# Performance work log

Hardware: AMD Instinct MI355X
Metric: run time of the kernel (lower is better)

## Reference

```python
import jax, jax.numpy as jnp
import numpy as np

B, T, D, V, L = 16, 1024, 512, 5000, 128
BLANK = 0
NEG = -1e30  # log-space 'zero' (avoid inf for stability)


def setup_inputs() -> dict:
    key = jax.random.key(0)
    k1, k2, k3, k4, k5 = jax.random.split(key, 5)
    hs_pad = jax.random.normal(k1, (B, T, D), jnp.float32)
    W = jax.random.normal(k2, (D, V), jnp.float32) * 0.02
    b = jnp.zeros((V,), jnp.float32)
    hlens = jax.random.randint(k3, (B,), T // 2, T + 1)          # frame lengths
    ys_lens = jax.random.randint(k4, (B,), 64, L + 1)             # label lengths
    ys_pad = jax.random.randint(k5, (B, L), 1, V)                 # labels, no blank
    return {"hs_pad": hs_pad, "hlens": hlens, "ys_pad": ys_pad,
            "ys_lens": ys_lens, "W": W, "b": b}


def _lse3(a, b, c):
    m = jnp.maximum(jnp.maximum(a, b), c)
    m = jnp.maximum(m, NEG)
    return m + jnp.log(jnp.exp(a - m) + jnp.exp(b - m) + jnp.exp(c - m))


def _ctc_loss(logp, hlens, ys_pad, ys_lens):
    # logp: (B, T, V) log-probabilities
    Bb, Tt, _ = logp.shape
    Ll = ys_pad.shape[1]
    S = 2 * Ll + 1
    # extended label sequence: blank, y1, blank, y2, ..., blank  -> (B, S)
    ext = jnp.full((Bb, S), BLANK, ys_pad.dtype).at[:, 1::2].set(ys_pad)
    # gather log-probs of extended labels: (B, T, S)
    lp_ext = jnp.take_along_axis(
        logp, jnp.broadcast_to(ext[:, None, :], (Bb, Tt, S)), axis=2)
    # skip transition from s-2 allowed iff ext[s] != blank and ext[s] != ext[s-2]
    ext_m2 = jnp.pad(ext[:, :-2], ((0, 0), (2, 0)), constant_values=-1)
    allow = (ext != BLANK) & (ext != ext_m2)  # (B, S)

    alpha0 = (jnp.full((Bb, S), NEG, logp.dtype)
              .at[:, 0].set(lp_ext[:, 0, 0])
              .at[:, 1].set(lp_ext[:, 0, 1]))

    def step(alpha, xs):
        lp_t, t = xs
        a1 = alpha
        a2 = jnp.pad(alpha[:, :-1], ((0, 0), (1, 0)), constant_values=NEG)
        a3 = jnp.where(allow,
                       jnp.pad(alpha[:, :-2], ((0, 0), (2, 0)), constant_values=NEG),
                       NEG)
        new = _lse3(a1, a2, a3) + lp_t
        keep = (t < hlens)[:, None]  # freeze alpha past each sequence length
        return jnp.where(keep, new, alpha), None

    lp_seq = jnp.swapaxes(lp_ext, 0, 1)  # (T, B, S)
    ts = jnp.arange(1, Tt)
    alpha, _ = jax.lax.scan(step, alpha0, (lp_seq[1:], ts))

    idx1 = 2 * ys_lens                 # final blank
    idx2 = jnp.maximum(idx1 - 1, 0)    # final label
    a_end = jnp.take_along_axis(alpha, jnp.stack([idx1, idx2], axis=1), axis=1)
    ll = jax.scipy.special.logsumexp(a_end, axis=1)  # (B,)
    loss = -ll
    loss = jnp.where(jnp.isfinite(loss) & (loss < 1e29), loss, 0.0)  # zero_infinity
    # reduction='sum', then normalize by total token count (normalize_length=True)
    return jnp.sum(loss) / jnp.sum(ys_lens).astype(logp.dtype)


def reference(hs_pad, hlens, ys_pad, ys_lens, W, b):
    logits = hs_pad @ W + b                      # (B, T, V), dropout_rate=0
    logp = jax.nn.log_softmax(logits, axis=2)    # same math as transpose->log_softmax
    return _ctc_loss(logp, hlens, ys_pad, ys_lens)
```

## Files before the change

### kernel.cpp

```cpp
#include <hip/hip_runtime.h>
#include <hip/hip_bf16.h>
#include <math.h>

#define B_   16
#define T_   1024
#define D_   512
#define V_   5000
#define VP_  5120
#define L_   128
#define S_   257
#define J_   129
#define JP_  160
#define M_   (B_*T_)
#define NT_  40
#define NEGF (-1e30f)
#define LOG2E_F 1.4426950408889634f

typedef __attribute__((ext_vector_type(8))) short short8;
typedef __attribute__((ext_vector_type(4))) float float4v;

__device__ inline void load_lds_16(const void* g, void* l) {
    __builtin_amdgcn_global_load_lds(
        (const __attribute__((address_space(1))) unsigned int*)g,
        (__attribute__((address_space(3))) unsigned int*)l, 16, 0, 0);
}

__device__ inline unsigned short f2bf(float f) {
    union { float f; unsigned int u; } x; x.f = f;
    unsigned int r = x.u + 0x7FFFu + ((x.u >> 16) & 1u);
    return (unsigned short)(r >> 16);
}

__device__ inline float wave_shr1_f32(float v) {
    return __int_as_float(__builtin_amdgcn_update_dpp(
        0, __float_as_int(v), 0x138, 0xF, 0xF, true));
}
__device__ inline int wave_shr1_i32(int v) {
    return __builtin_amdgcn_update_dpp(0, v, 0x138, 0xF, 0xF, true);
}

__global__ __launch_bounds__(256) void k_convert_hs(
    const float* __restrict__ hs, unsigned short* __restrict__ Ah)
{
    size_t base = ((size_t)blockIdx.x * 256 + threadIdx.x) * 8;
    float4 a = *(const float4*)&hs[base];
    float4 b = *(const float4*)&hs[base + 4];
    short8 o;
    o[0] = (short)f2bf(a.x); o[1] = (short)f2bf(a.y);
    o[2] = (short)f2bf(a.z); o[3] = (short)f2bf(a.w);
    o[4] = (short)f2bf(b.x); o[5] = (short)f2bf(b.y);
    o[6] = (short)f2bf(b.z); o[7] = (short)f2bf(b.w);
    *(short8*)&Ah[base] = o;
}

__global__ __launch_bounds__(256) void k_transpose_w(
    const float* __restrict__ W, unsigned short* __restrict__ Wt)
{
    __shared__ float tile[32][33];
    int v0 = blockIdx.x * 32, k0 = blockIdx.y * 32;
    int tx = threadIdx.x, ty = threadIdx.y;
#pragma unroll
    for (int r = 0; r < 4; r++) {
        int kk = r * 8 + ty;
        float val = 0.f;
        if (v0 + tx < V_) val = W[(size_t)(k0 + kk) * V_ + v0 + tx];
        tile[kk][tx] = val;
    }
    __syncthreads();
#pragma unroll
    for (int r = 0; r < 4; r++) {
        int vloc = r * 8 + ty;
        Wt[(size_t)(v0 + vloc) * D_ + k0 + tx] = f2bf(tile[tx][vloc]);
    }
}

__global__ __launch_bounds__(512) void k_gemm_lse_mfma(
    const unsigned short* __restrict__ Ah,
    const unsigned short* __restrict__ Wt,
    const float* __restrict__ bias,
    float* __restrict__ part_s)
{
    __shared__ unsigned short As[256 * 32];
    __shared__ unsigned short Bs[128 * 32];
    __shared__ float sm_s[2][256];

    const int bx = blockIdx.x;
    const int by = blockIdx.y;
    const int tid = threadIdx.x;
    const int rowBase = bx * 256, colBase = by * 128;
    const int lane = tid & 63, wv = tid >> 6;
    const int wi = wv >> 1, wj = wv & 1;
    const int g = lane >> 4, lo = lane & 15;
    const int cs = g ^ (lo & 3);

    float4v acc[4][4];
#pragma unroll
    for (int i = 0; i < 4; i++)
#pragma unroll
        for (int j = 0; j < 4; j++) acc[i][j] = (float4v){0.f, 0.f, 0.f, 0.f};

    for (int it = 0; it < 16; it++) {
        const int k0 = it * 32;
        __syncthreads();
#pragma unroll
        for (int l = 0; l < 3; l++) {
            int slot = tid + l * 512;
            if (slot < 1024) {
                int r = slot >> 2, q = slot & 3;
                int qs = q ^ (r & 3);
                load_lds_16(&Ah[(size_t)(rowBase + r) * D_ + k0 + qs * 8],
                            &As[r * 32 + q * 8]);
            } else {
                int s = slot - 1024;
                int r = s >> 2, q = s & 3;
                int qs = q ^ (r & 3);
                load_lds_16(&Wt[(size_t)(colBase + r) * D_ + k0 + qs * 8],
                            &Bs[r * 32 + q * 8]);
            }
        }
        __syncthreads();

        short8 a[4], b[4];
#pragma unroll
        for (int i = 0; i < 4; i++)
            a[i] = *(const short8*)&As[(wi * 64 + i * 16 + lo) * 32 + cs * 8];
#pragma unroll
        for (int j = 0; j < 4; j++)
            b[j] = *(const short8*)&Bs[(wj * 64 + j * 16 + lo) * 32 + cs * 8];
#pragma unroll
        for (int i = 0; i < 4; i++)
#pragma unroll
            for (int j = 0; j < 4; j++)
                acc[i][j] = __builtin_amdgcn_mfma_f32_16x16x32_bf16(
                    a[i], b[j], acc[i][j], 0, 0, 0);
    }

    float bj[4]; bool vj[4];
#pragma unroll
    for (int j = 0; j < 4; j++) {
        int col = colBase + wj * 64 + j * 16 + lo;
        vj[j] = (col < V_);
        bj[j] = vj[j] ? bias[col] : 0.f;
    }
#pragma unroll
    for (int i = 0; i < 4; i++) {
#pragma unroll
        for (int r = 0; r < 4; r++) {
            float s = 0.f;
#pragma unroll
            for (int j = 0; j < 4; j++)
                if (vj[j]) s += __expf(acc[i][j][r] + bj[j]);
#pragma unroll
            for (int off = 1; off < 16; off <<= 1)
                s += __shfl_xor(s, off, 16);
            if (lo == 0)
                sm_s[wj][wi * 64 + i * 16 + g * 4 + r] = s;
        }
    }
    __syncthreads();
    if (tid < 256)
        part_s[(size_t)(rowBase + tid) * NT_ + by] = sm_s[0][tid] + sm_s[1][tid];
}

__global__ __launch_bounds__(64) void k_gather_wb(
    const unsigned short* __restrict__ Wt,
    const float* __restrict__ bias,
    const int* __restrict__ ys,
    unsigned short* __restrict__ Wgb,
    float* __restrict__ bgb)
{
    int b = blockIdx.x, j = blockIdx.y;
    int lab = 0;
    if (j >= 1 && j <= L_) lab = ys[b * L_ + (j - 1)];
    else if (j > L_) lab = VP_ - 1;
    const unsigned short* src = &Wt[(size_t)lab * D_];
    unsigned short* dst = &Wgb[((size_t)b * JP_ + j) * D_];
    int t = threadIdx.x;
    *(short8*)&dst[t * 8] = *(const short8*)&src[t * 8];
    if (t == 0) bgb[b * JP_ + j] = (j <= L_) ? bias[lab] : 0.f;
}

__global__ __launch_bounds__(256) void k_label_mfma(
    const unsigned short* __restrict__ Ah,
    const unsigned short* __restrict__ Wgb,
    const float* __restrict__ bgb,
    const float* __restrict__ part_s,
    float* __restrict__ ll,
    float* __restrict__ lb2)
{
    __shared__ unsigned short As[64 * 32];
    __shared__ unsigned short Bs[JP_ * 32];
    __shared__ float outs[64][JP_ + 1];

    const int b = blockIdx.x, t0 = blockIdx.y * 64;
    const int tid = threadIdx.x;
    const int lane = tid & 63, w = tid >> 6;
    const int g = lane >> 4, lo = lane & 15;

    const unsigned short* Ab = Ah  + ((size_t)b * T_ + t0) * D_;
    const unsigned short* Bb = Wgb + (size_t)b * JP_ * D_;

    float4v acc[10];
#pragma unroll
    for (int j = 0; j < 10; j++) acc[j] = (float4v){0.f, 0.f, 0.f, 0.f};

    for (int it = 0; it < 16; it++) {
        const int k0 = it * 32;
        __syncthreads();
        {
            int r = tid >> 2, q = tid & 3;
            load_lds_16(&Ab[(size_t)r * D_ + k0 + q * 8], &As[r * 32 + q * 8]);
        }
        for (int s = tid; s < 640; s += 256) {
            int r = s >> 2, q = s & 3;
            load_lds_16(&Bb[(size_t)r * D_ + k0 + q * 8], &Bs[r * 32 + q * 8]);
        }
        __syncthreads();

        short8 a = *(const short8*)&As[(w * 16 + lo) * 32 + g * 8];
#pragma unroll
        for (int j = 0; j < 10; j++) {
            short8 bf = *(const short8*)&Bs[(j * 16 + lo) * 32 + g * 8];
            acc[j] = __builtin_amdgcn_mfma_f32_16x16x32_bf16(a, bf, acc[j], 0, 0, 0);
        }
    }

#pragma unroll
    for (int j = 0; j < 10; j++) {
        float bv = bgb[b * JP_ + j * 16 + lo];
#pragma unroll
        for (int r = 0; r < 4; r++)
            outs[w * 16 + g * 4 + r][j * 16 + lo] = acc[j][r] + bv;
    }
    __syncthreads();
    for (int idx = tid; idx < 64 * J_; idx += 256) {
        int r = idx / J_, j = idx - r * J_;
        float l0 = outs[r][0];
        float v  = outs[r][j];
        ll[((size_t)b * T_ + t0 + r) * J_ + j] = (j == 0) ? 1.f : __expf(v - l0);
    }
    if (tid < 64) {
        size_t row = (size_t)b * T_ + t0 + tid;
        const float* ps = &part_s[row * NT_];
        float s = 0.f;
#pragma unroll
        for (int i = 0; i < NT_; i++) s += ps[i];
        lb2[row] = (outs[tid][0] - __logf(s)) * LOG2E_F;
    }
}

#define CH_   32
#define CHB_  (CH_ * J_ * 4)
#define NLD_  ((CHB_ + 1023) / 1024)

__global__ __launch_bounds__(64, 1) void k_ctc_alpha(
    const float* __restrict__ Pr,
    const float* __restrict__ lb2,
    const int* __restrict__ hlens,
    const int* __restrict__ ys,
    const int* __restrict__ ys_lens,
    float* __restrict__ loss_b)
{
    __shared__ float llds[2][NLD_ * 256];
    __shared__ float fin_m[S_];
    __shared__ int   fin_e[S_];
    const int b = blockIdx.x;
    const int l = threadIdx.x;
    const int hl = hlens[b];
    const float* prb = Pr  + (size_t)b * T_ * J_;
    const float* lbb = lb2 + (size_t)b * T_;

    double acc = 0.0;
    for (int tt = l; tt < hl; tt += 64) acc += (double)lbb[tt];
#pragma unroll
    for (int off = 32; off > 0; off >>= 1)
        acc += __shfl_xor(acc, off, 64);

    float u1f = 0.f, u3f;
    {
        const int* yb = ys + b * L_;
        if (l >= 1) u1f = (yb[2 * l] != yb[2 * l - 1]) ? 1.f : 0.f;
        u3f = (yb[2 * l + 1] != yb[2 * l]) ? 1.f : 0.f;
    }
    const int c1 = 2 * l + 1;

    float a0 = (l == 0) ? 1.f : 0.f;
    float a1 = (l == 0) ? prb[1] : 0.f;
    float a2 = 0.f, a3 = 0.f, a4 = 0.f;
    int   E  = 0;
    float fl   = (l == 0) ? 0.f : 1.f;
    float u1fl = u1f * fl;

#define RENORM() do {                                                         \
        float mx_ = fmaxf(fmaxf(fmaxf(a0, a1), fmaxf(a2, a3)), a4);           \
        unsigned long long act_ = __ballot(mx_ > 0.f);                        \
        int La_ = 63 - __builtin_clzll(act_);           \
        if (mx_ > 0.f) {                                                      \
            int e_ = (int)((__float_as_uint(mx_) >> 23) & 255u) - 127;        \
            a0 = ldexpf(a0, -e_); a1 = ldexpf(a1, -e_); a2 = ldexpf(a2, -e_); \
            a3 = ldexpf(a3, -e_); a4 = ldexpf(a4, -e_);                       \
            E += e_;                                                          \
        }                                                                     \
        int Ea_ = __shfl(E, La_, 64);                                         \
        if (!(mx_ > 0.f)) E = Ea_;                   \
        int Ep_ = wave_shr1_i32(E);                                           \
        int dE_ = Ep_ - E;                                                    \
        dE_ = dE_ > 126 ? 126 : (dE_ < -126 ? -126 : dE_);                    \
        fl = (l == 0) ? 0.f : ldexpf(1.f, dE_);                               \
        u1fl = u1f * fl;                                                      \
    } while (0)

#define STEP_P(p1_, p3_) do {                                                 \
        float prev_ = wave_shr1_f32(a3);                                      \
        float n0_ = fmaf(prev_, fl, a0);                                      \
        float n1_ = fmaf(prev_, u1fl, a0 + a1) * (p1_);                       \
        float n2_ = a2 + a1;                                                  \
        float n3_ = fmaf(a1, u3f, a3 + a2) * (p3_);                           \
        float n4_ = a4 + a3;                                                  \
        a0 = n0_; a1 = n1_; a2 = n2_; a3 = n3_; a4 = n4_;                     \
    } while (0)

    {
        const char* src = (const char*)prb;
        char* dst = (char*)&llds[0][0];
#pragma unroll
        for (int k = 0; k < NLD_; k++)
            load_lds_16(src + (size_t)k * 1024 + (size_t)l * 16, dst + k * 1024);
    }

    const int nch = (hl + CH_ - 1) / CH_;
    int t = 1;
    for (int c = 0; c < nch; c++) {
        asm volatile("s_waitcnt vmcnt(0)" ::: "memory");
        __builtin_amdgcn_sched_barrier(0);
        if (c + 1 < nch) {
            const char* src = (const char*)(prb + (size_t)(c + 1) * CH_ * J_);
            char* dst = (char*)&llds[(c + 1) & 1][0];
#pragma unroll
            for (int k = 0; k < NLD_; k++)
                load_lds_16(src + (size_t)k * 1024 + (size_t)l * 16, dst + k * 1024);
        }
        const float* lbuf = &llds[c & 1][0];
        const int cbase = c * CH_;
        const int tcap = (hl < cbase + CH_) ? hl : cbase + CH_;
        const int tmid = (tcap < cbase + 16) ? tcap : cbase + 16;
#pragma unroll
        for (int half = 0; half < 2; half++) {
            const int tlim = (half == 0) ? tmid : tcap;
            while (t + 8 <= tlim) {
                float pv1[8], pv3[8];
#pragma unroll
                for (int i = 0; i < 8; i++) {
                    int r = t + i - cbase;
                    pv1[i] = lbuf[r * J_ + c1];
                    pv3[i] = lbuf[r * J_ + c1 + 1];
                }
#pragma unroll
                for (int i = 0; i < 8; i++) STEP_P(pv1[i], pv3[i]);
                t += 8;
            }
            while (t < tlim) {
                int r = t - cbase;
                float p1 = lbuf[r * J_ + c1];
                float p3 = lbuf[r * J_ + c1 + 1];
                STEP_P(p1, p3);
                t++;
            }
            RENORM();
        }
    }

    fin_m[4 * l + 0] = a0; fin_m[4 * l + 1] = a1;
    fin_m[4 * l + 2] = a2; fin_m[4 * l + 3] = a3;
    fin_e[4 * l + 0] = E;  fin_e[4 * l + 1] = E;
    fin_e[4 * l + 2] = E;  fin_e[4 * l + 3] = E;
    if (l == 63) { fin_m[256] = a4; fin_e[256] = E; }
    __syncthreads();

    if (l == 0) {
        int yl = ys_lens[b];
        int i1 = 2 * yl;
        int i2 = (i1 > 0) ? i1 - 1 : 0;
        int Ea = fin_e[i1], Eb = fin_e[i2];
        int Em = Ea > Eb ? Ea : Eb;
        int da = Ea - Em, db = Eb - Em;
        da = da < -126 ? -126 : da;  db = db < -126 ? -126 : db;
        float v = ldexpf(fin_m[i1], da) + ldexpf(fin_m[i2], db);
        float lg = __log2f(v) + (float)Em;
        double lln = ((double)lg + acc) * 0.6931471805599453;
        float loss = -(float)lln;
        if (!isfinite(loss) || loss >= 1e29f) loss = 0.f;
        loss_b[b] = loss;
    }
#undef RENORM
#undef STEP_P
}

__global__ void k_final(const float* __restrict__ loss_b,
                        const int* __restrict__ ys_lens,
                        float* __restrict__ out)
{
    int t = threadIdx.x;
    float v = (t < B_) ? loss_b[t] : 0.f;
    int   n = (t < B_) ? ys_lens[t] : 0;
    for (int off = 32; off > 0; off >>= 1) {
        v += __shfl_down(v, off, 64);
        n += __shfl_down(n, off, 64);
    }
    if (t == 0) out[0] = v / (float)n;
}

extern "C" void kernel_launch(void* const* d_in, const int* in_sizes, int n_in,
                              void* d_out, int out_size, void* d_ws, size_t ws_size,
                              hipStream_t stream)
{
    const float* hs      = (const float*)d_in[0];
    const int*   hlens   = (const int*)  d_in[1];
    const int*   ys      = (const int*)  d_in[2];
    const int*   ys_lens = (const int*)  d_in[3];
    const float* W       = (const float*)d_in[4];
    const float* bias    = (const float*)d_in[5];
    float* out = (float*)d_out;

    float* ws = (float*)d_ws;
    float* part_s = ws;
    unsigned short* Wgb = (unsigned short*)(part_s + (size_t)M_ * NT_);
    float* bgb    = (float*)(Wgb + (size_t)B_ * JP_ * D_);
    float* llab   = bgb    + (size_t)B_ * JP_;
    float* loss_b = llab   + (size_t)B_ * T_ * J_;
    float* lb2    = loss_b + 16;
    unsigned short* Ah = (unsigned short*)(lb2 + M_);
    unsigned short* Wt = Ah + (size_t)M_ * D_;

    k_convert_hs<<<(M_ * D_) / (256 * 8), 256, 0, stream>>>(hs, Ah);
    k_transpose_w<<<dim3(VP_ / 32, D_ / 32), dim3(32, 8), 0, stream>>>(W, Wt);
    k_gemm_lse_mfma<<<dim3(M_ / 256, NT_), 512, 0, stream>>>(Ah, Wt, bias, part_s);
    k_gather_wb<<<dim3(B_, JP_), 64, 0, stream>>>(Wt, bias, ys, Wgb, bgb);
    k_label_mfma<<<dim3(B_, T_ / 64), 256, 0, stream>>>(Ah, Wgb, bgb, part_s, llab, lb2);
    k_ctc_alpha<<<B_, 64, 0, stream>>>(llab, lb2, hlens, ys, ys_lens, loss_b);
    k_final<<<1, 64, 0, stream>>>(loss_b, ys_lens, out);
}
```

Before: 263.0 us.

## Pack eight CTC alpha waves per block and finalize via wave shuffles

The CTC alpha recursion kernel now runs eight independent batch sequences as eight waves inside each 512-thread block, launching 2 blocks instead of 16 single-wave blocks. Each wave has its own double-buffered LDS staging area, and the chunk size drops from 32 to 16 timesteps, with one renormalisation per chunk, to fit the larger LDS footprint. The final alpha lookup now uses cross-lane shuffles instead of writing to shared memory and synchronising. This packs the work onto fewer CUs, which could slow the latency-bound per-wave recursion through shared SIMD and LDS contention and more frequent renormalisation.

```diff
diff --git a/kernel.cpp b/kernel.cpp
--- a/kernel.cpp
+++ b/kernel.cpp
@@ -249,11 +249,10 @@
     }
 }
 
-#define CH_   32
-#define CHB_  (CH_ * J_ * 4)
-#define NLD_  ((CHB_ + 1023) / 1024)
-
-__global__ __launch_bounds__(64, 1) void k_ctc_alpha(
+#define CH_   16
+#define NLD_  9
+
+__global__ __launch_bounds__(512, 1) void k_ctc_alpha(
     const float* __restrict__ Pr,
     const float* __restrict__ lb2,
     const int* __restrict__ hlens,
@@ -261,11 +260,10 @@
     const int* __restrict__ ys_lens,
     float* __restrict__ loss_b)
 {
-    __shared__ float llds[2][NLD_ * 256];
-    __shared__ float fin_m[S_];
-    __shared__ int   fin_e[S_];
-    const int b = blockIdx.x;
-    const int l = threadIdx.x;
+    __shared__ float llds[8][2][NLD_ * 256];
+    const int w = threadIdx.x >> 6;
+    const int l = threadIdx.x & 63;
+    const int b = blockIdx.x * 8 + w;
     const int hl = hlens[b];
     const float* prb = Pr  + (size_t)b * T_ * J_;
     const float* lbb = lb2 + (size_t)b * T_;
@@ -322,7 +320,7 @@
 
     {
         const char* src = (const char*)prb;
-        char* dst = (char*)&llds[0][0];
+        char* dst = (char*)&llds[w][0][0];
 #pragma unroll
         for (int k = 0; k < NLD_; k++)
             load_lds_16(src + (size_t)k * 1024 + (size_t)l * 16, dst + k * 1024);
@@ -335,57 +333,54 @@
         __builtin_amdgcn_sched_barrier(0);
         if (c + 1 < nch) {
             const char* src = (const char*)(prb + (size_t)(c + 1) * CH_ * J_);
-            char* dst = (char*)&llds[(c + 1) & 1][0];
+            char* dst = (char*)&llds[w][(c + 1) & 1][0];
 #pragma unroll
             for (int k = 0; k < NLD_; k++)
                 load_lds_16(src + (size_t)k * 1024 + (size_t)l * 16, dst + k * 1024);
         }
-        const float* lbuf = &llds[c & 1][0];
+        const float* lbuf = &llds[w][c & 1][0];
         const int cbase = c * CH_;
         const int tcap = (hl < cbase + CH_) ? hl : cbase + CH_;
-        const int tmid = (tcap < cbase + 16) ? tcap : cbase + 16;
-#pragma unroll
-        for (int half = 0; half < 2; half++) {
-            const int tlim = (half == 0) ? tmid : tcap;
-            while (t + 8 <= tlim) {
-                float pv1[8], pv3[8];
-#pragma unroll
-                for (int i = 0; i < 8; i++) {
-                    int r = t + i - cbase;
-                    pv1[i] = lbuf[r * J_ + c1];
-                    pv3[i] = lbuf[r * J_ + c1 + 1];
-                }
-#pragma unroll
-                for (int i = 0; i < 8; i++) STEP_P(pv1[i], pv3[i]);
-                t += 8;
+        while (t + 8 <= tcap) {
+            float pv1[8], pv3[8];
+#pragma unroll
+            for (int i = 0; i < 8; i++) {
+                int r = t + i - cbase;
+                pv1[i] = lbuf[r * J_ + c1];
+                pv3[i] = lbuf[r * J_ + c1 + 1];
             }
-            while (t < tlim) {
-                int r = t - cbase;
-                float p1 = lbuf[r * J_ + c1];
-                float p3 = lbuf[r * J_ + c1 + 1];
-                STEP_P(p1, p3);
-                t++;
-            }
-            RENORM();
-        }
-    }
-
-    fin_m[4 * l + 0] = a0; fin_m[4 * l + 1] = a1;
-    fin_m[4 * l + 2] = a2; fin_m[4 * l + 3] = a3;
-    fin_e[4 * l + 0] = E;  fin_e[4 * l + 1] = E;
-    fin_e[4 * l + 2] = E;  fin_e[4 * l + 3] = E;
-    if (l == 63) { fin_m[256] = a4; fin_e[256] = E; }
-    __syncthreads();
+#pragma unroll
+            for (int i = 0; i < 8; i++) STEP_P(pv1[i], pv3[i]);
+            t += 8;
+        }
+        while (t < tcap) {
+            int r = t - cbase;
+            float p1 = lbuf[r * J_ + c1];
+            float p3 = lbuf[r * J_ + c1 + 1];
+            STEP_P(p1, p3);
+            t++;
+        }
+        RENORM();
+    }
+
+    int yl = ys_lens[b];
+    int i1 = 2 * yl, i2 = i1 - 1;
+    int ln1 = (i1 >= 256) ? 63 : (i1 >> 2);
+    int sl1 = (i1 >= 256) ? 4  : (i1 & 3);
+    float cand1 = (sl1 == 0) ? a0 : (sl1 == 1) ? a1 : (sl1 == 2) ? a2
+                : (sl1 == 3) ? a3 : a4;
+    float m1 = __shfl(cand1, ln1, 64);
+    int   E1 = __shfl(E, ln1, 64);
+    int ln2 = i2 >> 2, sl2 = i2 & 3;
+    float cand2 = (sl2 == 0) ? a0 : (sl2 == 1) ? a1 : (sl2 == 2) ? a2 : a3;
+    float m2 = __shfl(cand2, ln2, 64);
+    int   E2 = __shfl(E, ln2, 64);
 
     if (l == 0) {
-        int yl = ys_lens[b];
-        int i1 = 2 * yl;
-        int i2 = (i1 > 0) ? i1 - 1 : 0;
-        int Ea = fin_e[i1], Eb = fin_e[i2];
-        int Em = Ea > Eb ? Ea : Eb;
-        int da = Ea - Em, db = Eb - Em;
-        da = da < -126 ? -126 : da;  db = db < -126 ? -126 : db;
-        float v = ldexpf(fin_m[i1], da) + ldexpf(fin_m[i2], db);
+        int Em = E1 > E2 ? E1 : E2;
+        int d1 = E1 - Em, d2 = E2 - Em;
+        d1 = d1 < -126 ? -126 : d1;  d2 = d2 < -126 ? -126 : d2;
+        float v = ldexpf(m1, d1) + ldexpf(m2, d2);
         float lg = __log2f(v) + (float)Em;
         double lln = ((double)lg + acc) * 0.6931471805599453;
         float loss = -(float)lln;
@@ -437,6 +432,6 @@
     k_gemm_lse_mfma<<<dim3(M_ / 256, NT_), 512, 0, stream>>>(Ah, Wt, bias, part_s);
     k_gather_wb<<<dim3(B_, JP_), 64, 0, stream>>>(Wt, bias, ys, Wgb, bgb);
     k_label_mfma<<<dim3(B_, T_ / 64), 256, 0, stream>>>(Ah, Wgb, bgb, part_s, llab, lb2);
-    k_ctc_alpha<<<B_, 64, 0, stream>>>(llab, lb2, hlens, ys, ys_lens, loss_b);
+    k_ctc_alpha<<<2, 512, 0, stream>>>(llab, lb2, hlens, ys, ys_lens, loss_b);
     k_final<<<1, 64, 0, stream>>>(loss_b, ys_lens, out);
 }
```

After: 275.9 us. +4.9%, slower.
